# Optimization experiments

Measured on AMD Instinct MI355X. Metric: run time of the kernel, lower is better.

Reference implementation:

```python
import jax, jax.numpy as jnp
import numpy as np

B, S, D = 2, 2048, 1024
H, DH = 16, 64
LN_EPS = 1e-5
NEG_INF = -1e9


def setup_inputs() -> dict:
    key = jax.random.key(0)
    ks = jax.random.split(key, 8)
    x = jax.random.normal(ks[0], (B, S, D), dtype=jnp.float32)
    mask = jax.random.randint(ks[1], (B, 1, S, S), 0, 5) == 0
    sc = 1.0 / np.sqrt(D)
    W_attn = jax.random.normal(ks[2], (D, 3 * H * DH), dtype=jnp.float32) * sc
    b_attn = jnp.zeros((3 * H * DH,), dtype=jnp.float32)
    W_out = jax.random.normal(ks[3], (H * DH, D), dtype=jnp.float32) * sc
    b_out = jnp.zeros((D,), dtype=jnp.float32)
    ln_g = jnp.ones((D,), dtype=jnp.float32)
    ln_b = jnp.zeros((D,), dtype=jnp.float32)
    return {"x": x, "W_attn": W_attn, "b_attn": b_attn, "W_out": W_out,
            "b_out": b_out, "ln_g": ln_g, "ln_b": ln_b, "mask": mask}


def reference(x, W_attn, b_attn, W_out, b_out, ln_g, ln_b, mask):
    bs, s, _ = x.shape
    qkv = x @ W_attn + b_attn                      # [b, s, 3*H*DH]
    q, k, v = jnp.split(qkv, 3, axis=-1)
    q = q.reshape(bs, s, H, DH)
    k = k.reshape(bs, s, H, DH)
    v = v.reshape(bs, s, H, DH)
    scores = jnp.einsum('bqhd,bkhd->bhqk', q, k) / np.sqrt(DH)
    scores = jnp.where(mask, NEG_INF, scores)
    probs = jax.nn.softmax(scores, axis=-1)        # attn_p = 0 -> dropout is identity
    attn = jnp.einsum('bhqk,bkhd->bqhd', probs, v).reshape(bs, s, H * DH)
    y = x + (attn @ W_out + b_out)                 # resid_p = 0
    mu = jnp.mean(y, axis=-1, keepdims=True)
    var = jnp.mean((y - mu) ** 2, axis=-1, keepdims=True)
    return (y - mu) * jax.lax.rsqrt(var + LN_EPS) * ln_g + ln_b
```

## Files before the change

kernel.cpp:

```cpp
#include <hip/hip_runtime.h>
#include <math.h>

#define BB 2
#define SS 2048
#define DD 1024
#define HH 16
#define DHD 64
#define N3 3072
#define LN_EPS 1e-5f

#define PLANE (BB*HH*SS*DHD)

typedef __attribute__((ext_vector_type(8))) short bf16x8;
typedef __attribute__((ext_vector_type(4))) float f32x4;
typedef unsigned int u32;
typedef unsigned short ushort_t;

static __device__ __forceinline__ short f2bf(float f) {
  union { float f; unsigned u; } a;
  a.f = f;
  unsigned r = a.u + 0x7fffu + ((a.u >> 16) & 1u);
  return (short)(r >> 16);
}

static __device__ __forceinline__ u32 fbits(float f) {
  union { float f; u32 u; } a; a.f = f; return a.u;
}

static __device__ __forceinline__ void gload_lds16(const void* g, void* l) {
  __builtin_amdgcn_global_load_lds(
      (const __attribute__((address_space(1))) u32*)g,
      (__attribute__((address_space(3))) u32*)l, 16, 0, 0);
}

#define PREP_CONV_B   2048
#define PREP_TA_B     768
#define PREP_TO_B     256
#define PREP_PACK_B   32768
#define PREP_TOTAL_B  (PREP_CONV_B + PREP_TA_B + PREP_TO_B + PREP_PACK_B)

__global__ __launch_bounds__(256) void prep_kernel(
    const float* __restrict__ x, ushort_t* __restrict__ xb,
    const float* __restrict__ Wa, ushort_t* __restrict__ watt,
    const float* __restrict__ Wo, ushort_t* __restrict__ wot,
    const int* __restrict__ mask, unsigned long long* __restrict__ bits) {
  __shared__ float tile[64][65];
  const int tid = threadIdx.x;
  const int bid = blockIdx.x;

  if (bid < PREP_CONV_B) {
    int i = (bid * 256 + tid) * 8;
    float4 a = *(const float4*)&x[i];
    float4 b = *(const float4*)&x[i + 4];
    short s[8] = {f2bf(a.x), f2bf(a.y), f2bf(a.z), f2bf(a.w),
                  f2bf(b.x), f2bf(b.y), f2bf(b.z), f2bf(b.w)};
    *(bf16x8*)&xb[i] = *(bf16x8*)s;
    return;
  }
  if (bid < PREP_CONV_B + PREP_TA_B + PREP_TO_B) {
    const float* W; ushort_t* Wt; int K, N, nb, kb;
    if (bid < PREP_CONV_B + PREP_TA_B) {
      int idx = bid - PREP_CONV_B;
      W = Wa; Wt = watt; K = DD; N = N3;
      nb = (idx % 48) * 64; kb = (idx / 48) * 64;
    } else {
      int idx = bid - PREP_CONV_B - PREP_TA_B;
      W = Wo; Wt = wot; K = DD; N = DD;
      nb = (idx % 16) * 64; kb = (idx / 16) * 64;
    }
    #pragma unroll
    for (int i = 0; i < 4; ++i) {
      int idx = tid + i * 256;
      int r = idx >> 4, c = (idx & 15) * 4;
      float4 v = *(const float4*)&W[(size_t)(kb + r) * N + nb + c];
      tile[r][c] = v.x; tile[r][c + 1] = v.y;
      tile[r][c + 2] = v.z; tile[r][c + 3] = v.w;
    }
    __syncthreads();
    #pragma unroll
    for (int i = 0; i < 4; ++i) {
      int idx = tid + i * 256;
      int n = idx >> 4, k = (idx & 15) * 4;
      short4 s;
      s.x = f2bf(tile[k][n]); s.y = f2bf(tile[k + 1][n]);
      s.z = f2bf(tile[k + 2][n]); s.w = f2bf(tile[k + 3][n]);
      *(short4*)&Wt[(size_t)(nb + n) * K + kb + k] = s;
    }
    return;
  }
  {
    size_t g = (size_t)(bid - PREP_CONV_B - PREP_TA_B - PREP_TO_B) * 256 + tid;
    int m = mask[g];
    unsigned long long b = __ballot(m != 0);
    if ((tid & 63) == 0) bits[g >> 6] = b;
  }
}

#define GEMM_MAIN(Aptr, Btptr, Kdim)                                          \
  __shared__ ushort_t As[128 * 64];                                           \
  __shared__ ushort_t Bs[128 * 64];                                           \
  const int tid = threadIdx.x;                                                \
  const int wave = tid >> 6, lane = tid & 63;                                 \
  const int lane16 = lane & 15, quad = lane >> 4;                             \
  const int wm = wave & 1, wn = wave >> 1;                                    \
  const int bm = blockIdx.y * 128, bn = blockIdx.x * 128;                     \
  const int srow = lane >> 3;                                                 \
  const int sg = (lane & 7) ^ srow;                                           \
  f32x4 acc[4][4];                                                            \
  _Pragma("unroll") for (int i = 0; i < 4; ++i)                               \
    _Pragma("unroll") for (int j = 0; j < 4; ++j)                             \
      acc[i][j] = (f32x4){0.f, 0.f, 0.f, 0.f};                                \
  const ushort_t* agp[4];                                                     \
  const ushort_t* bgp[4];                                                     \
  _Pragma("unroll") for (int i = 0; i < 4; ++i) {                             \
    int seg = wave * 4 + i;                                                   \
    int r = seg * 8 + srow;                                                   \
    agp[i] = Aptr + (size_t)(bm + r) * Kdim + sg * 8;                         \
    bgp[i] = Btptr + (size_t)(bn + r) * Kdim + sg * 8;                        \
  }                                                                           \
  for (int k0 = 0; k0 < Kdim; k0 += 64) {                                     \
    _Pragma("unroll") for (int i = 0; i < 4; ++i) {                           \
      int seg = wave * 4 + i;                                                 \
      gload_lds16(agp[i] + k0, &As[seg * 512]);                               \
      gload_lds16(bgp[i] + k0, &Bs[seg * 512]);                               \
    }                                                                         \
    __syncthreads();                                                          \
    _Pragma("unroll") for (int ks = 0; ks < 2; ++ks) {                        \
      bf16x8 af[4], bfr[4];                                                   \
      _Pragma("unroll") for (int mt = 0; mt < 4; ++mt) {                      \
        int ra = wm * 64 + mt * 16 + lane16;                                  \
        int kc = ks * 4 + quad;                                               \
        af[mt] = *(const bf16x8*)&As[ra * 64 + ((kc ^ (ra & 7)) * 8)];        \
      }                                                                       \
      _Pragma("unroll") for (int nt = 0; nt < 4; ++nt) {                      \
        int rb = wn * 64 + nt * 16 + lane16;                                  \
        int kc = ks * 4 + quad;                                               \
        bfr[nt] = *(const bf16x8*)&Bs[rb * 64 + ((kc ^ (rb & 7)) * 8)];       \
      }                                                                       \
      _Pragma("unroll") for (int mt = 0; mt < 4; ++mt)                        \
        _Pragma("unroll") for (int nt = 0; nt < 4; ++nt)                      \
          acc[mt][nt] = __builtin_amdgcn_mfma_f32_16x16x32_bf16(              \
              af[mt], bfr[nt], acc[mt][nt], 0, 0, 0);                         \
    }                                                                         \
    __syncthreads();                                                          \
  }

__global__ __launch_bounds__(256) void gemm_qkv_mfma(
    const ushort_t* __restrict__ A, const ushort_t* __restrict__ Bt,
    const float* __restrict__ bias, ushort_t* __restrict__ qkvh) {
  GEMM_MAIN(A, Bt, DD)
  #pragma unroll
  for (int nt = 0; nt < 4; ++nt) {
    int col = bn + wn * 64 + nt * 16 + lane16;
    int which = col >> 10, hcol = col & 1023;
    int head = hcol >> 6, d = hcol & 63;
    float bv = bias[col];
    ushort_t* plane = qkvh + (size_t)which * PLANE;
    #pragma unroll
    for (int mt = 0; mt < 4; ++mt) {
      #pragma unroll
      for (int reg = 0; reg < 4; ++reg) {
        int row = bm + wm * 64 + mt * 16 + quad * 4 + reg;
        int bb = row >> 11, ss = row & (SS - 1);
        plane[((size_t)(bb * HH + head) * SS + ss) * DHD + d] =
            (ushort_t)f2bf(acc[mt][nt][reg] + bv);
      }
    }
  }
}

__global__ __launch_bounds__(256) void gemm_proj_mfma(
    const ushort_t* __restrict__ A, const ushort_t* __restrict__ Bt,
    const float* __restrict__ bias, const float* __restrict__ xres,
    float* __restrict__ Y) {
  GEMM_MAIN(A, Bt, DD)
  #pragma unroll
  for (int nt = 0; nt < 4; ++nt) {
    int col = bn + wn * 64 + nt * 16 + lane16;
    float bv = bias[col];
    #pragma unroll
    for (int mt = 0; mt < 4; ++mt) {
      #pragma unroll
      for (int reg = 0; reg < 4; ++reg) {
        int row = bm + wm * 64 + mt * 16 + quad * 4 + reg;
        Y[(size_t)row * DD + col] =
            acc[mt][nt][reg] + bv + xres[(size_t)row * DD + col];
      }
    }
  }
}

__global__ __launch_bounds__(512) void attn_mfma_kernel(
    const ushort_t* __restrict__ qh, const ushort_t* __restrict__ kh,
    const ushort_t* __restrict__ vh, const u32* __restrict__ mbits,
    ushort_t* __restrict__ attn_out) {
  __shared__ __align__(16) short Kt[2][64][76];
  __shared__ __align__(16) short Vt[2][64][76];
  __shared__ __align__(16) short Pt[8][16][76];

  const int tid = threadIdx.x;
  const int wave = tid >> 6, lane = tid & 63;
  const int lane16 = lane & 15, quad = lane >> 4;

  const int bh = blockIdx.x & 31;
  const int qt = blockIdx.x >> 5;
  const int bbi = bh >> 4, hhi = bh & 15;
  const size_t head_base = (size_t)bh * SS * DHD;
  const int q0 = qt * 128 + wave * 16;
  const int qrow_g = q0 + quad * 4;

  bf16x8 qf[2];
  {
    const float kScale = 0.125f * 1.44269504f;
    const ushort_t* qsrc = &qh[head_base + (size_t)(q0 + lane16) * DHD + quad * 8];
    #pragma unroll
    for (int ks = 0; ks < 2; ++ks) {
      bf16x8 r = *(const bf16x8*)&qsrc[ks * 32];
      #pragma unroll
      for (int e = 0; e < 8; ++e) {
        union { u32 u; float f; } c;
        c.u = ((u32)(ushort_t)r[e]) << 16;
        c.f *= kScale;
        r[e] = f2bf(c.f);
      }
      qf[ks] = r;
    }
  }

  bf16x8 onesf;
  #pragma unroll
  for (int e = 0; e < 8; ++e) onesf[e] = (short)0x3F80;

  f32x4 acc[4];
  f32x4 lacc = (f32x4){0.f, 0.f, 0.f, 0.f};
  #pragma unroll
  for (int dt = 0; dt < 4; ++dt) acc[dt] = (f32x4){0.f, 0.f, 0.f, 0.f};

  const u32* mrow = mbits + ((size_t)(bbi * SS) + q0 + lane16) * 64;
  const int shq = quad * 4;

  const int kg_r = tid >> 3;
  const int kg_c = (tid & 7) * 8;
  const int vs_c = tid & 63;
  const int v_half = wave >> 2;
  const int vs_rb_l = (wave & 3) * 16;
  const int vs_rb_g = wave * 16;

  bf16x8 kreg[2];
  short4 vreg[4];
  uint4 mwn;
  {
    #pragma unroll
    for (int i = 0; i < 2; ++i)
      kreg[i] = *(const bf16x8*)&kh[head_base + (size_t)(kg_r + i * 64) * DHD + kg_c];
    #pragma unroll
    for (int i = 0; i < 4; ++i) {
      int r0 = vs_rb_g + i * 4;
      const ushort_t* vsrc = &vh[head_base + (size_t)r0 * DHD + vs_c];
      vreg[i].x = (short)vsrc[0];
      vreg[i].y = (short)vsrc[DHD];
      vreg[i].z = (short)vsrc[2 * DHD];
      vreg[i].w = (short)vsrc[3 * DHD];
    }
    mwn = *(const uint4*)&mrow[0];
  }

  for (int kt = 0; kt < SS; kt += 128) {
    __syncthreads();
    #pragma unroll
    for (int i = 0; i < 2; ++i)
      *(bf16x8*)&Kt[i][kg_r][kg_c] = kreg[i];
    #pragma unroll
    for (int i = 0; i < 4; ++i)
      *(short4*)&Vt[v_half][vs_c][vs_rb_l + i * 4] = vreg[i];
    uint4 mwc = mwn;
    __syncthreads();

    const int kt2 = kt + 128;
    if (kt2 < SS) {
      #pragma unroll
      for (int i = 0; i < 2; ++i)
        kreg[i] = *(const bf16x8*)&kh[head_base + (size_t)(kt2 + kg_r + i * 64) * DHD + kg_c];
      #pragma unroll
      for (int i = 0; i < 4; ++i) {
        int r0 = kt2 + vs_rb_g + i * 4;
        const ushort_t* vsrc = &vh[head_base + (size_t)r0 * DHD + vs_c];
        vreg[i].x = (short)vsrc[0];
        vreg[i].y = (short)vsrc[DHD];
        vreg[i].z = (short)vsrc[2 * DHD];
        vreg[i].w = (short)vsrc[3 * DHD];
      }
      mwn = *(const uint4*)&mrow[kt2 >> 5];
    }

    #pragma unroll
    for (int h = 0; h < 2; ++h) {
      f32x4 sc[4];
      #pragma unroll
      for (int nt = 0; nt < 4; ++nt) {
        sc[nt] = (f32x4){0.f, 0.f, 0.f, 0.f};
        #pragma unroll
        for (int ks = 0; ks < 2; ++ks) {
          bf16x8 kf = *(const bf16x8*)&Kt[h][nt * 16 + lane16][ks * 32 + quad * 8];
          sc[nt] = __builtin_amdgcn_mfma_f32_16x16x32_bf16(kf, qf[ks], sc[nt], 0, 0, 0);
        }
      }

      const u32 wlo = h ? mwc.z : mwc.x;
      const u32 whi = h ? mwc.w : mwc.y;
      const u32 tl = wlo >> shq;
      const u32 th = whi >> shq;
      #pragma unroll
      for (int nt = 0; nt < 4; ++nt) {
        const u32 w = (nt & 2) ? th : tl;
        const u32 base = (nt & 1) ? 0x10000u : 1u;
        float e0 = (w & (base << 0)) ? 0.f : exp2f(sc[nt][0]);
        float e1 = (w & (base << 1)) ? 0.f : exp2f(sc[nt][1]);
        float e2 = (w & (base << 2)) ? 0.f : exp2f(sc[nt][2]);
        float e3 = (w & (base << 3)) ? 0.f : exp2f(sc[nt][3]);
        u32 w0 = __builtin_amdgcn_perm(fbits(e1) + 0x8000u, fbits(e0) + 0x8000u,
                                       0x07060302u);
        u32 w1 = __builtin_amdgcn_perm(fbits(e3) + 0x8000u, fbits(e2) + 0x8000u,
                                       0x07060302u);
        uint2 pw; pw.x = w0; pw.y = w1;
        *(uint2*)&Pt[wave][lane16][nt * 16 + shq] = pw;
      }

      #pragma unroll
      for (int ks = 0; ks < 2; ++ks) {
        bf16x8 pf = *(const bf16x8*)&Pt[wave][lane16][ks * 32 + quad * 8];
        lacc = __builtin_amdgcn_mfma_f32_16x16x32_bf16(pf, onesf, lacc, 0, 0, 0);
        #pragma unroll
        for (int dt = 0; dt < 4; ++dt) {
          bf16x8 vf = *(const bf16x8*)&Vt[h][dt * 16 + lane16][ks * 32 + quad * 8];
          acc[dt] = __builtin_amdgcn_mfma_f32_16x16x32_bf16(pf, vf, acc[dt], 0, 0, 0);
        }
      }
    }
  }

  #pragma unroll
  for (int reg = 0; reg < 4; ++reg) {
    float inv = 1.0f / lacc[reg];
    ushort_t* orow = &attn_out[((size_t)(bbi * SS) + qrow_g + reg) * DD
                               + hhi * DHD + lane16];
    #pragma unroll
    for (int dt = 0; dt < 4; ++dt)
      orow[dt * 16] = (ushort_t)f2bf(acc[dt][reg] * inv);
  }
}

__global__ __launch_bounds__(256) void ln_kernel(
    float* __restrict__ Y, const float* __restrict__ g,
    const float* __restrict__ bta) {
  const int r = blockIdx.x;
  const int tid = threadIdx.x;
  float4 v = *(const float4*)&Y[(size_t)r * DD + tid * 4];
  float sum = v.x + v.y + v.z + v.w;
  float sq = v.x * v.x + v.y * v.y + v.z * v.z + v.w * v.w;
  #pragma unroll
  for (int off = 32; off; off >>= 1) {
    sum += __shfl_down(sum, off);
    sq += __shfl_down(sq, off);
  }
  __shared__ float ps[4], pq[4];
  __shared__ float mu_s, rs_s;
  const int wave = tid >> 6;
  if ((tid & 63) == 0) { ps[wave] = sum; pq[wave] = sq; }
  __syncthreads();
  if (tid == 0) {
    float s = ps[0] + ps[1] + ps[2] + ps[3];
    float qq = pq[0] + pq[1] + pq[2] + pq[3];
    float mu = s * (1.0f / DD);
    float var = qq * (1.0f / DD) - mu * mu;
    mu_s = mu;
    rs_s = rsqrtf(var + LN_EPS);
  }
  __syncthreads();
  const float mu = mu_s, rs = rs_s;
  float4 g4 = *(const float4*)&g[tid * 4];
  float4 b4 = *(const float4*)&bta[tid * 4];
  float4 ov;
  ov.x = (v.x - mu) * rs * g4.x + b4.x;
  ov.y = (v.y - mu) * rs * g4.y + b4.y;
  ov.z = (v.z - mu) * rs * g4.z + b4.z;
  ov.w = (v.w - mu) * rs * g4.w + b4.w;
  *(float4*)&Y[(size_t)r * DD + tid * 4] = ov;
}

extern "C" void kernel_launch(void* const* d_in, const int* in_sizes, int n_in,
                              void* d_out, int out_size, void* d_ws, size_t ws_size,
                              hipStream_t stream) {
  const float* x      = (const float*)d_in[0];
  const float* W_attn = (const float*)d_in[1];
  const float* b_attn = (const float*)d_in[2];
  const float* W_out  = (const float*)d_in[3];
  const float* b_out  = (const float*)d_in[4];
  const float* ln_g   = (const float*)d_in[5];
  const float* ln_b   = (const float*)d_in[6];
  const int*   mask   = (const int*)d_in[7];
  float* out = (float*)d_out;
  ushort_t* ws = (ushort_t*)d_ws;

  ushort_t* xb    = ws;
  ushort_t* watt  = xb + (size_t)BB * SS * DD;
  ushort_t* wot   = watt + (size_t)N3 * DD;
  ushort_t* qh    = wot + (size_t)DD * DD;
  ushort_t* kh    = qh + (size_t)PLANE;
  ushort_t* vh    = kh + (size_t)PLANE;
  ushort_t* attnb = vh + (size_t)PLANE;
  u32* mbits      = (u32*)(attnb + (size_t)BB * SS * DD);

  prep_kernel<<<dim3(PREP_TOTAL_B), 256, 0, stream>>>(
      x, xb, W_attn, watt, W_out, wot, mask, (unsigned long long*)mbits);

  gemm_qkv_mfma<<<dim3(N3 / 128, (BB * SS) / 128), 256, 0, stream>>>(
      xb, watt, b_attn, qh);
  attn_mfma_kernel<<<dim3(BB * HH * (SS / 128)), 512, 0, stream>>>(
      qh, kh, vh, mbits, attnb);
  gemm_proj_mfma<<<dim3(DD / 128, (BB * SS) / 128), 256, 0, stream>>>(
      attnb, wot, b_out, x, out);
  ln_kernel<<<dim3(BB * SS), 256, 0, stream>>>(out, ln_g, ln_b);
}
```

Before: 256.2 us.

## Pre-transpose V and stream K/V tiles directly into swizzled LDS

Adds a kernel that transposes V into a per-head [d][s] layout, writing into the no-longer-needed xb buffer. The attention kernel now stages 64-key K and V tiles with direct global-to-LDS loads into XOR-swizzled, double-buffered shared memory, and needs only one barrier per tile. This replaces the register-staged, strided scalar V gathers and padded LDS arrays. The aim is to cut global load inefficiency and LDS bank conflicts and to overlap loads with MFMA work, at the cost of an extra kernel launch and extra V traffic.

Measured after the change: 262.7 us. +2.6%, slower.

```diff
diff --git a/kernel.cpp b/kernel.cpp
--- a/kernel.cpp
+++ b/kernel.cpp
@@ -190,12 +190,38 @@
   }
 }
 
+__global__ __launch_bounds__(256) void vtrans_kernel(
+    const ushort_t* __restrict__ vh, ushort_t* __restrict__ vt) {
+  __shared__ short t[64][80];
+  const int tid = threadIdx.x;
+  const int bh = blockIdx.x >> 5;
+  const int st = blockIdx.x & 31;
+  const size_t hb = (size_t)bh * SS * DHD;
+  #pragma unroll
+  for (int i = 0; i < 2; ++i) {
+    int idx = tid + i * 256;
+    int r = idx >> 3, ch = idx & 7;
+    bf16x8 v = *(const bf16x8*)&vh[hb + (size_t)(st * 64 + r) * DHD + ch * 8];
+    *(bf16x8*)&t[r][ch * 8] = v;
+  }
+  __syncthreads();
+  #pragma unroll
+  for (int i = 0; i < 2; ++i) {
+    int idx = tid + i * 256;
+    int d = idx >> 3, ch = idx & 7;
+    short s[8];
+    #pragma unroll
+    for (int j = 0; j < 8; ++j) s[j] = t[ch * 8 + j][d];
+    *(bf16x8*)&vt[hb + (size_t)d * SS + st * 64 + ch * 8] = *(bf16x8*)s;
+  }
+}
+
 __global__ __launch_bounds__(512) void attn_mfma_kernel(
     const ushort_t* __restrict__ qh, const ushort_t* __restrict__ kh,
-    const ushort_t* __restrict__ vh, const u32* __restrict__ mbits,
+    const ushort_t* __restrict__ vt, const u32* __restrict__ mbits,
     ushort_t* __restrict__ attn_out) {
-  __shared__ __align__(16) short Kt[2][64][76];
-  __shared__ __align__(16) short Vt[2][64][76];
+  __shared__ __align__(16) ushort_t Ks[2][64 * 64];
+  __shared__ __align__(16) ushort_t Vs[2][64 * 64];
   __shared__ __align__(16) short Pt[8][16][76];
 
   const int tid = threadIdx.x;
@@ -239,104 +265,74 @@
   const u32* mrow = mbits + ((size_t)(bbi * SS) + q0 + lane16) * 64;
   const int shq = quad * 4;
 
-  const int kg_r = tid >> 3;
-  const int kg_c = (tid & 7) * 8;
-  const int vs_c = tid & 63;
-  const int v_half = wave >> 2;
-  const int vs_rb_l = (wave & 3) * 16;
-  const int vs_rb_g = wave * 16;
-
-  bf16x8 kreg[2];
-  short4 vreg[4];
-  uint4 mwn;
-  {
-    #pragma unroll
-    for (int i = 0; i < 2; ++i)
-      kreg[i] = *(const bf16x8*)&kh[head_base + (size_t)(kg_r + i * 64) * DHD + kg_c];
-    #pragma unroll
-    for (int i = 0; i < 4; ++i) {
-      int r0 = vs_rb_g + i * 4;
-      const ushort_t* vsrc = &vh[head_base + (size_t)r0 * DHD + vs_c];
-      vreg[i].x = (short)vsrc[0];
-      vreg[i].y = (short)vsrc[DHD];
-      vreg[i].z = (short)vsrc[2 * DHD];
-      vreg[i].w = (short)vsrc[3 * DHD];
-    }
-    mwn = *(const uint4*)&mrow[0];
-  }
-
-  for (int kt = 0; kt < SS; kt += 128) {
-    __syncthreads();
-    #pragma unroll
-    for (int i = 0; i < 2; ++i)
-      *(bf16x8*)&Kt[i][kg_r][kg_c] = kreg[i];
-    #pragma unroll
-    for (int i = 0; i < 4; ++i)
-      *(short4*)&Vt[v_half][vs_c][vs_rb_l + i * 4] = vreg[i];
-    uint4 mwc = mwn;
-    __syncthreads();
-
-    const int kt2 = kt + 128;
-    if (kt2 < SS) {
-      #pragma unroll
-      for (int i = 0; i < 2; ++i)
-        kreg[i] = *(const bf16x8*)&kh[head_base + (size_t)(kt2 + kg_r + i * 64) * DHD + kg_c];
-      #pragma unroll
-      for (int i = 0; i < 4; ++i) {
-        int r0 = kt2 + vs_rb_g + i * 4;
-        const ushort_t* vsrc = &vh[head_base + (size_t)r0 * DHD + vs_c];
-        vreg[i].x = (short)vsrc[0];
-        vreg[i].y = (short)vsrc[DHD];
-        vreg[i].z = (short)vsrc[2 * DHD];
-        vreg[i].w = (short)vsrc[3 * DHD];
-      }
-      mwn = *(const uint4*)&mrow[kt2 >> 5];
-    }
-
-    #pragma unroll
-    for (int h = 0; h < 2; ++h) {
-      f32x4 sc[4];
-      #pragma unroll
-      for (int nt = 0; nt < 4; ++nt) {
-        sc[nt] = (f32x4){0.f, 0.f, 0.f, 0.f};
-        #pragma unroll
-        for (int ks = 0; ks < 2; ++ks) {
-          bf16x8 kf = *(const bf16x8*)&Kt[h][nt * 16 + lane16][ks * 32 + quad * 8];
-          sc[nt] = __builtin_amdgcn_mfma_f32_16x16x32_bf16(kf, qf[ks], sc[nt], 0, 0, 0);
-        }
-      }
-
-      const u32 wlo = h ? mwc.z : mwc.x;
-      const u32 whi = h ? mwc.w : mwc.y;
-      const u32 tl = wlo >> shq;
-      const u32 th = whi >> shq;
-      #pragma unroll
-      for (int nt = 0; nt < 4; ++nt) {
-        const u32 w = (nt & 2) ? th : tl;
-        const u32 base = (nt & 1) ? 0x10000u : 1u;
-        float e0 = (w & (base << 0)) ? 0.f : exp2f(sc[nt][0]);
-        float e1 = (w & (base << 1)) ? 0.f : exp2f(sc[nt][1]);
-        float e2 = (w & (base << 2)) ? 0.f : exp2f(sc[nt][2]);
-        float e3 = (w & (base << 3)) ? 0.f : exp2f(sc[nt][3]);
-        u32 w0 = __builtin_amdgcn_perm(fbits(e1) + 0x8000u, fbits(e0) + 0x8000u,
-                                       0x07060302u);
-        u32 w1 = __builtin_amdgcn_perm(fbits(e3) + 0x8000u, fbits(e2) + 0x8000u,
-                                       0x07060302u);
-        uint2 pw; pw.x = w0; pw.y = w1;
-        *(uint2*)&Pt[wave][lane16][nt * 16 + shq] = pw;
-      }
-
+  const int sr = tid >> 3;
+  const int sc_ = tid & 7;
+  const int scsrc = sc_ ^ (sr & 7);
+  const ushort_t* kstage = kh + head_base + (size_t)sr * DHD + scsrc * 8;
+  const ushort_t* vstage = vt + head_base + (size_t)sr * SS + scsrc * 8;
+  const int sdst = wave * 512;
+
+  const int swz = (lane16 & 7);
+
+  gload_lds16(kstage, &Ks[0][sdst]);
+  gload_lds16(vstage, &Vs[0][sdst]);
+  uint2 mcur = *(const uint2*)&mrow[0];
+  __syncthreads();
+
+  const int NTILES = SS / 64;
+  for (int t = 0; t < NTILES; ++t) {
+    const int cur = t & 1;
+    uint2 mnext = mcur;
+    if (t + 1 < NTILES) {
+      gload_lds16(kstage + (size_t)(t + 1) * 64 * DHD, &Ks[cur ^ 1][sdst]);
+      gload_lds16(vstage + (t + 1) * 64, &Vs[cur ^ 1][sdst]);
+      mnext = *(const uint2*)&mrow[(t + 1) * 2];
+    }
+
+    f32x4 sc[4];
+    #pragma unroll
+    for (int nt = 0; nt < 4; ++nt) {
+      sc[nt] = (f32x4){0.f, 0.f, 0.f, 0.f};
       #pragma unroll
       for (int ks = 0; ks < 2; ++ks) {
-        bf16x8 pf = *(const bf16x8*)&Pt[wave][lane16][ks * 32 + quad * 8];
-        lacc = __builtin_amdgcn_mfma_f32_16x16x32_bf16(pf, onesf, lacc, 0, 0, 0);
-        #pragma unroll
-        for (int dt = 0; dt < 4; ++dt) {
-          bf16x8 vf = *(const bf16x8*)&Vt[h][dt * 16 + lane16][ks * 32 + quad * 8];
-          acc[dt] = __builtin_amdgcn_mfma_f32_16x16x32_bf16(pf, vf, acc[dt], 0, 0, 0);
-        }
+        int rk = nt * 16 + lane16;
+        bf16x8 kf = *(const bf16x8*)&Ks[cur][rk * 64 + (((ks * 4 + quad) ^ swz) * 8)];
+        sc[nt] = __builtin_amdgcn_mfma_f32_16x16x32_bf16(kf, qf[ks], sc[nt], 0, 0, 0);
       }
     }
+
+    const u32 tl = mcur.x >> shq;
+    const u32 th = mcur.y >> shq;
+    #pragma unroll
+    for (int nt = 0; nt < 4; ++nt) {
+      const u32 w = (nt & 2) ? th : tl;
+      const u32 base = (nt & 1) ? 0x10000u : 1u;
+      float e0 = (w & (base << 0)) ? 0.f : exp2f(sc[nt][0]);
+      float e1 = (w & (base << 1)) ? 0.f : exp2f(sc[nt][1]);
+      float e2 = (w & (base << 2)) ? 0.f : exp2f(sc[nt][2]);
+      float e3 = (w & (base << 3)) ? 0.f : exp2f(sc[nt][3]);
+      u32 w0 = __builtin_amdgcn_perm(fbits(e1) + 0x8000u, fbits(e0) + 0x8000u,
+                                     0x07060302u);
+      u32 w1 = __builtin_amdgcn_perm(fbits(e3) + 0x8000u, fbits(e2) + 0x8000u,
+                                     0x07060302u);
+      uint2 pw; pw.x = w0; pw.y = w1;
+      *(uint2*)&Pt[wave][lane16][nt * 16 + shq] = pw;
+    }
+
+    #pragma unroll
+    for (int ks = 0; ks < 2; ++ks) {
+      bf16x8 pf = *(const bf16x8*)&Pt[wave][lane16][ks * 32 + quad * 8];
+      lacc = __builtin_amdgcn_mfma_f32_16x16x32_bf16(pf, onesf, lacc, 0, 0, 0);
+      #pragma unroll
+      for (int dt = 0; dt < 4; ++dt) {
+        int rv = dt * 16 + lane16;
+        bf16x8 vf = *(const bf16x8*)&Vs[cur][rv * 64 + (((ks * 4 + quad) ^ swz) * 8)];
+        acc[dt] = __builtin_amdgcn_mfma_f32_16x16x32_bf16(pf, vf, acc[dt], 0, 0, 0);
+      }
+    }
+
+    mcur = mnext;
+    __syncthreads();
   }
 
   #pragma unroll
@@ -410,14 +406,16 @@
   ushort_t* vh    = kh + (size_t)PLANE;
   ushort_t* attnb = vh + (size_t)PLANE;
   u32* mbits      = (u32*)(attnb + (size_t)BB * SS * DD);
+  ushort_t* vtb   = xb;
 
   prep_kernel<<<dim3(PREP_TOTAL_B), 256, 0, stream>>>(
       x, xb, W_attn, watt, W_out, wot, mask, (unsigned long long*)mbits);
 
   gemm_qkv_mfma<<<dim3(N3 / 128, (BB * SS) / 128), 256, 0, stream>>>(
       xb, watt, b_attn, qh);
+  vtrans_kernel<<<dim3(BB * HH * (SS / 64)), 256, 0, stream>>>(vh, vtb);
   attn_mfma_kernel<<<dim3(BB * HH * (SS / 128)), 512, 0, stream>>>(
-      qh, kh, vh, mbits, attnb);
+      qh, kh, vtb, mbits, attnb);
   gemm_proj_mfma<<<dim3(DD / 128, (BB * SS) / 128), 256, 0, stream>>>(
       attnb, wot, b_out, x, out);
   ln_kernel<<<dim3(BB * SS), 256, 0, stream>>>(out, ln_g, ln_b);
```
